# Performance work log

Hardware: AMD Instinct MI355X
Metric: run time of the kernel (lower is better)

Reference implementation:

```python
import jax, jax.numpy as jnp
import numpy as np

DIM = 128  # matches init kwarg `dim`; scale = dim ** 0.5


def setup_inputs() -> dict:
    key = jax.random.key(0)
    k1, k2, k3, k4 = jax.random.split(key, 4)
    A = 100000
    K = 1600000  # num edges
    z_msg_all = jax.random.normal(k1, (A, DIM), dtype=jnp.float32)
    recv_query_all = jax.random.normal(k2, (A, DIM), dtype=jnp.float32)
    i_idx = jax.random.randint(k3, (K,), 0, A, dtype=jnp.int64)
    j_idx = jax.random.randint(k4, (K,), 0, A, dtype=jnp.int64)
    return {"z_msg_all": z_msg_all, "recv_query_all": recv_query_all,
            "i_idx": i_idx, "j_idx": j_idx, "A": A}


def reference(z_msg_all, recv_query_all, i_idx, j_idx, A):
    # q_j = z[j], k_i = z[i]; per-edge scores; segmented softmax over recipient j;
    # weighted scatter-add of values k_i into pooled[j]. recv_query_all is unused
    # in the original forward (kept for signature fidelity).
    scale = DIM ** 0.5
    k = z_msg_all[i_idx]                     # (K, D) gather
    q = z_msg_all[j_idx]                     # (K, D) gather
    scores = jnp.sum(q * k, axis=-1) / scale  # (K,)
    # segmented softmax (3-pass: amax, exp, sum)
    max_per = jax.ops.segment_max(scores, j_idx, num_segments=A)  # (A,)
    exp = jnp.exp(scores - max_per[j_idx])                         # (K,)
    denom = jax.ops.segment_sum(exp, j_idx, num_segments=A)        # (A,)
    alpha = exp / (denom[j_idx] + 1e-6)                            # (K,)
    # weighted scatter-add of values into recipients
    pooled = jax.ops.segment_sum(alpha[:, None] * k, j_idx, num_segments=A)  # (A, D)
    return pooled
```

## Files before the change

kernel.cpp:

```cpp
#include <hip/hip_runtime.h>
#include <math.h>


typedef _Float16 h2 __attribute__((ext_vector_type(2)));

#define CAP   8192
#define ABLK  512
#define EPB   2048

__device__ inline h2 as_h2(unsigned u) { return __builtin_bit_cast(h2, u); }

__global__ __launch_bounds__(ABLK) void bin_kernel(
        const float* __restrict__ z, uint4* __restrict__ z16,
        const int* __restrict__ i_idx, const int* __restrict__ j_idx,
        int* __restrict__ gcount, unsigned* __restrict__ binned,
        int n16, int K, int NB) {
    int tid = threadIdx.x;

    {
        const float4* __restrict__ z4 = reinterpret_cast<const float4*>(z);
        int nth = gridDim.x * ABLK;
        for (int t = blockIdx.x * ABLK + tid; t < n16; t += nth) {
            float4 a = z4[(size_t)2 * t];
            float4 c = z4[(size_t)2 * t + 1];
            uint4 o;
            o.x = __builtin_bit_cast(unsigned, __builtin_amdgcn_cvt_pkrtz(a.x, a.y));
            o.y = __builtin_bit_cast(unsigned, __builtin_amdgcn_cvt_pkrtz(a.z, a.w));
            o.z = __builtin_bit_cast(unsigned, __builtin_amdgcn_cvt_pkrtz(c.x, c.y));
            o.w = __builtin_bit_cast(unsigned, __builtin_amdgcn_cvt_pkrtz(c.z, c.w));
            z16[t] = o;
        }
    }

    __shared__ int lhist[ABLK];
    __shared__ int loff[ABLK + 1];
    __shared__ int lcur[ABLK];
    __shared__ int gbase[ABLK];
    __shared__ unsigned staged_p[EPB];
    __shared__ unsigned short staged_b[EPB];

    lhist[tid] = 0;
    __syncthreads();

    int ebase = blockIdx.x * EPB;
    int myi[4], myj[4], myb[4];
    #pragma unroll
    for (int q = 0; q < 4; ++q) {
        int e = ebase + tid + q * ABLK;
        if (e < K) {
            myj[q] = j_idx[e];
            myi[q] = i_idx[e];
            myb[q] = myj[q] >> 8;
            atomicAdd(&lhist[myb[q]], 1);
        } else {
            myb[q] = -1;
        }
    }
    __syncthreads();
    for (int off = 1; off < ABLK; off <<= 1) {
        int v = (tid >= off) ? lhist[tid - off] : 0;
        __syncthreads();
        lhist[tid] += v;
        __syncthreads();
    }
    loff[tid + 1] = lhist[tid];
    if (tid == 0) loff[0] = 0;
    __syncthreads();
    int cntb = loff[tid + 1] - loff[tid];
    if (tid < NB && cntb > 0)
        gbase[tid] = tid * CAP + atomicAdd(&gcount[tid], cntb);
    lcur[tid] = loff[tid];
    __syncthreads();
    #pragma unroll
    for (int q = 0; q < 4; ++q) {
        if (myb[q] >= 0) {
            int p = atomicAdd(&lcur[myb[q]], 1);
            staged_p[p] = ((unsigned)myi[q] << 8) | ((unsigned)myj[q] & 255u);
            staged_b[p] = (unsigned short)myb[q];
        }
    }
    __syncthreads();
    int totE = loff[ABLK];
    for (int idx = tid; idx < totE; idx += ABLK) {
        int bb = staged_b[idx];
        binned[(size_t)gbase[bb] + (idx - loff[bb])] = staged_p[idx];
    }
}

__global__ __launch_bounds__(512) void finish_kernel(
        unsigned* __restrict__ binned, const int* __restrict__ gcount,
        int2* __restrict__ seg, int A) {
    __shared__ unsigned staged[CAP];
    __shared__ int hist[256];
    __shared__ int offs[257];
    __shared__ int cur[256];

    int b = blockIdx.x;
    int tid = threadIdx.x;
    int cnt = gcount[b];
    if (cnt > CAP) cnt = CAP;
    unsigned* __restrict__ src = binned + (size_t)b * CAP;

    if (tid < 256) hist[tid] = 0;
    for (int x = tid; x < cnt; x += 512) staged[x] = src[x];
    __syncthreads();
    for (int x = tid; x < cnt; x += 512)
        atomicAdd(&hist[staged[x] & 255u], 1);
    __syncthreads();
    for (int off = 1; off < 256; off <<= 1) {
        int v = 0;
        if (tid < 256 && tid >= off) v = hist[tid - off];
        __syncthreads();
        if (tid < 256 && tid >= off) hist[tid] += v;
        __syncthreads();
    }
    if (tid == 0) offs[0] = 0;
    if (tid < 256) offs[tid + 1] = hist[tid];
    __syncthreads();
    if (tid < 256) cur[tid] = offs[tid];
    __syncthreads();
    for (int x = tid; x < cnt; x += 512) {
        unsigned pk = staged[x];
        int p = atomicAdd(&cur[pk & 255u], 1);
        src[p] = pk >> 8;
    }
    if (tid < 256) {
        int j = (b << 8) + tid;
        if (j < A)
            seg[j] = make_int2(b * CAP + offs[tid], b * CAP + offs[tid + 1]);
    }
}

__global__ __launch_bounds__(256, 8) void attn_kernel(
        const uint4* __restrict__ zk,
        const unsigned* __restrict__ sorted_i, const int2* __restrict__ seg,
        float* __restrict__ out, int A) {
    int w = blockIdx.x * 4 + (threadIdx.x >> 6);
    if (w >= A) return;
    int lane = threadIdx.x & 63;
    int g = lane >> 3;
    int r = lane & 7;

    const float kscale = 0.08838834764831843f * 1.4426950408889634f;

    uint4 uq0 = zk[(size_t)w * 16 + r];
    uint4 uq1 = zk[(size_t)w * 16 + 8 + r];
    h2 qh[8];
    qh[0] = as_h2(uq0.x); qh[1] = as_h2(uq0.y);
    qh[2] = as_h2(uq0.z); qh[3] = as_h2(uq0.w);
    qh[4] = as_h2(uq1.x); qh[5] = as_h2(uq1.y);
    qh[6] = as_h2(uq1.z); qh[7] = as_h2(uq1.w);

    int2 s01 = seg[w];

    float l = 0.0f;
    float acc[16];
    #pragma unroll
    for (int d = 0; d < 16; ++d) acc[d] = 0.0f;

    int p = s01.x + g;
    int i_next = (int)sorted_i[p];
    while (p < s01.y) {
        int i = i_next;
        i_next = (int)sorted_i[p + 8];
        uint4 u0 = zk[(size_t)i * 16 + r];
        uint4 u1 = zk[(size_t)i * 16 + 8 + r];
        h2 kh[8];
        kh[0] = as_h2(u0.x); kh[1] = as_h2(u0.y);
        kh[2] = as_h2(u0.z); kh[3] = as_h2(u0.w);
        kh[4] = as_h2(u1.x); kh[5] = as_h2(u1.y);
        kh[6] = as_h2(u1.z); kh[7] = as_h2(u1.w);

        float pa = __builtin_amdgcn_fdot2(qh[0], kh[0], 0.0f, false);
        float pb = __builtin_amdgcn_fdot2(qh[4], kh[4], 0.0f, false);
        pa = __builtin_amdgcn_fdot2(qh[1], kh[1], pa, false);
        pb = __builtin_amdgcn_fdot2(qh[5], kh[5], pb, false);
        pa = __builtin_amdgcn_fdot2(qh[2], kh[2], pa, false);
        pb = __builtin_amdgcn_fdot2(qh[6], kh[6], pb, false);
        pa = __builtin_amdgcn_fdot2(qh[3], kh[3], pa, false);
        pb = __builtin_amdgcn_fdot2(qh[7], kh[7], pb, false);
        float part = pa + pb;
        part += __shfl_xor(part, 1);
        part += __shfl_xor(part, 2);
        part += __shfl_xor(part, 4);

        float pe = exp2f(part * kscale);
        l += pe;
        #pragma unroll
        for (int t = 0; t < 8; ++t) {
            acc[2 * t]     = fmaf(pe, (float)kh[t].x, acc[2 * t]);
            acc[2 * t + 1] = fmaf(pe, (float)kh[t].y, acc[2 * t + 1]);
        }
        p += 8;
    }

    l += __shfl_xor(l, 8);
    l += __shfl_xor(l, 16);
    l += __shfl_xor(l, 32);

    {
        bool hi = (g & 4) != 0;
        #pragma unroll
        for (int t = 0; t < 4; ++t) {
            float sx = hi ? acc[2 * t]     : acc[2 * t + 8];
            float sy = hi ? acc[2 * t + 1] : acc[2 * t + 9];
            float rx = __shfl_xor(sx, 32);
            float ry = __shfl_xor(sy, 32);
            float kx = hi ? acc[2 * t + 8] : acc[2 * t];
            float ky = hi ? acc[2 * t + 9] : acc[2 * t + 1];
            acc[2 * t]     = kx + rx;
            acc[2 * t + 1] = ky + ry;
        }
        hi = (g & 2) != 0;
        #pragma unroll
        for (int t = 0; t < 2; ++t) {
            float sx = hi ? acc[2 * t]     : acc[2 * t + 4];
            float sy = hi ? acc[2 * t + 1] : acc[2 * t + 5];
            float rx = __shfl_xor(sx, 16);
            float ry = __shfl_xor(sy, 16);
            float kx = hi ? acc[2 * t + 4] : acc[2 * t];
            float ky = hi ? acc[2 * t + 5] : acc[2 * t + 1];
            acc[2 * t]     = kx + rx;
            acc[2 * t + 1] = ky + ry;
        }
        hi = (g & 1) != 0;
        {
            float sx = hi ? acc[0] : acc[2];
            float sy = hi ? acc[1] : acc[3];
            float rx = __shfl_xor(sx, 8);
            float ry = __shfl_xor(sy, 8);
            float kx = hi ? acc[2] : acc[0];
            float ky = hi ? acc[3] : acc[1];
            acc[0] = kx + rx;
            acc[1] = ky + ry;
        }
    }

    float inv = 1.0f / (l + 1e-6f);
    float2 o;
    o.x = acc[0] * inv;
    o.y = acc[1] * inv;
    int o_idx = ((g & 4) << 3) + 4 * r + (g & 3);
    reinterpret_cast<float2*>(out)[(size_t)w * 64 + o_idx] = o;
}

extern "C" void kernel_launch(void* const* d_in, const int* in_sizes, int n_in,
                              void* d_out, int out_size, void* d_ws, size_t ws_size,
                              hipStream_t stream) {
    const float* z     = (const float*)d_in[0];
    const int*   i_idx = (const int*)d_in[2];
    const int*   j_idx = (const int*)d_in[3];

    const int D = 128;
    int A = in_sizes[0] / D;
    int K = in_sizes[2];
    int n16 = A * (D / 8);
    int NB = (A + 255) >> 8;

    unsigned short* z16 = (unsigned short*)d_ws;
    unsigned* binned = (unsigned*)(z16 + (size_t)A * 128);
    int2* seg = (int2*)(binned + (size_t)NB * CAP);
    int* gcount = (int*)(seg + A);

    float* out = (float*)d_out;

    (void)hipMemsetAsync(gcount, 0, (size_t)NB * sizeof(int), stream);
    bin_kernel<<<(K + EPB - 1) / EPB, ABLK, 0, stream>>>(
        z, (uint4*)z16, i_idx, j_idx, gcount, binned, n16, K, NB);
    finish_kernel<<<NB, 512, 0, stream>>>(binned, gcount, seg, A);
    attn_kernel<<<(A + 3) / 4, 256, 0, stream>>>((const uint4*)z16, binned,
                                                 seg, out, A);
}
```

Baseline: 119.7 us.

## Deepen attn gather prefetch, double edges per bin block, widen finish sort

The attention loop now software-pipelines the fp16 key-row gather one iteration ahead and prefetches the index two iterations ahead, clamping indices so the speculative loads stay in bounds. The binning kernel handles 8 edges per thread instead of 4, uses an unrolled fixed-count conversion loop, and is sized so its grid also covers the fp32-to-fp16 conversion. The finish kernel runs 1024 threads and sorts into shared memory before a coalesced write-back, replacing scattered global writes. These changes aim to hide gather latency and cut launch/scatter costs, at the price of more registers in the attention kernel and more shared memory in finish.

Result: faster. 104.3 us (-12.9%).

```diff
diff --git a/kernel.cpp b/kernel.cpp
--- a/kernel.cpp
+++ b/kernel.cpp
@@ -6,7 +6,7 @@
 
 #define CAP   8192
 #define ABLK  512
-#define EPB   2048
+#define EPB   (ABLK * 8)
 
 __device__ inline h2 as_h2(unsigned u) { return __builtin_bit_cast(h2, u); }
 
@@ -16,19 +16,24 @@
         int* __restrict__ gcount, unsigned* __restrict__ binned,
         int n16, int K, int NB) {
     int tid = threadIdx.x;
+    int t0 = blockIdx.x * ABLK + tid;
+    int nth = gridDim.x * ABLK;
 
     {
         const float4* __restrict__ z4 = reinterpret_cast<const float4*>(z);
-        int nth = gridDim.x * ABLK;
-        for (int t = blockIdx.x * ABLK + tid; t < n16; t += nth) {
-            float4 a = z4[(size_t)2 * t];
-            float4 c = z4[(size_t)2 * t + 1];
-            uint4 o;
-            o.x = __builtin_bit_cast(unsigned, __builtin_amdgcn_cvt_pkrtz(a.x, a.y));
-            o.y = __builtin_bit_cast(unsigned, __builtin_amdgcn_cvt_pkrtz(a.z, a.w));
-            o.z = __builtin_bit_cast(unsigned, __builtin_amdgcn_cvt_pkrtz(c.x, c.y));
-            o.w = __builtin_bit_cast(unsigned, __builtin_amdgcn_cvt_pkrtz(c.z, c.w));
-            z16[t] = o;
+        #pragma unroll
+        for (int q = 0; q < 8; ++q) {
+            int t = t0 + q * nth;
+            if (t < n16) {
+                float4 a = z4[(size_t)2 * t];
+                float4 c = z4[(size_t)2 * t + 1];
+                uint4 o;
+                o.x = __builtin_bit_cast(unsigned, __builtin_amdgcn_cvt_pkrtz(a.x, a.y));
+                o.y = __builtin_bit_cast(unsigned, __builtin_amdgcn_cvt_pkrtz(a.z, a.w));
+                o.z = __builtin_bit_cast(unsigned, __builtin_amdgcn_cvt_pkrtz(c.x, c.y));
+                o.w = __builtin_bit_cast(unsigned, __builtin_amdgcn_cvt_pkrtz(c.z, c.w));
+                z16[t] = o;
+            }
         }
     }
 
@@ -43,9 +48,9 @@
     __syncthreads();
 
     int ebase = blockIdx.x * EPB;
-    int myi[4], myj[4], myb[4];
+    int myi[8], myj[8], myb[8];
     #pragma unroll
-    for (int q = 0; q < 4; ++q) {
+    for (int q = 0; q < 8; ++q) {
         int e = ebase + tid + q * ABLK;
         if (e < K) {
             myj[q] = j_idx[e];
@@ -72,7 +77,7 @@
     lcur[tid] = loff[tid];
     __syncthreads();
     #pragma unroll
-    for (int q = 0; q < 4; ++q) {
+    for (int q = 0; q < 8; ++q) {
         if (myb[q] >= 0) {
             int p = atomicAdd(&lcur[myb[q]], 1);
             staged_p[p] = ((unsigned)myi[q] << 8) | ((unsigned)myj[q] & 255u);
@@ -87,10 +92,11 @@
     }
 }
 
-__global__ __launch_bounds__(512) void finish_kernel(
+__global__ __launch_bounds__(1024) void finish_kernel(
         unsigned* __restrict__ binned, const int* __restrict__ gcount,
         int2* __restrict__ seg, int A) {
     __shared__ unsigned staged[CAP];
+    __shared__ int sorted_loc[CAP];
     __shared__ int hist[256];
     __shared__ int offs[257];
     __shared__ int cur[256];
@@ -102,9 +108,9 @@
     unsigned* __restrict__ src = binned + (size_t)b * CAP;
 
     if (tid < 256) hist[tid] = 0;
-    for (int x = tid; x < cnt; x += 512) staged[x] = src[x];
-    __syncthreads();
-    for (int x = tid; x < cnt; x += 512)
+    for (int x = tid; x < cnt; x += 1024) staged[x] = src[x];
+    __syncthreads();
+    for (int x = tid; x < cnt; x += 1024)
         atomicAdd(&hist[staged[x] & 255u], 1);
     __syncthreads();
     for (int off = 1; off < 256; off <<= 1) {
@@ -119,11 +125,13 @@
     __syncthreads();
     if (tid < 256) cur[tid] = offs[tid];
     __syncthreads();
-    for (int x = tid; x < cnt; x += 512) {
+    for (int x = tid; x < cnt; x += 1024) {
         unsigned pk = staged[x];
         int p = atomicAdd(&cur[pk & 255u], 1);
-        src[p] = pk >> 8;
-    }
+        sorted_loc[p] = (int)(pk >> 8);
+    }
+    __syncthreads();
+    for (int x = tid; x < cnt; x += 1024) src[x] = (unsigned)sorted_loc[x];
     if (tid < 256) {
         int j = (b << 8) + tid;
         if (j < A)
@@ -159,12 +167,19 @@
     for (int d = 0; d < 16; ++d) acc[d] = 0.0f;
 
     int p = s01.x + g;
-    int i_next = (int)sorted_i[p];
+    unsigned i0 = sorted_i[p];
+    i0 = (i0 < (unsigned)A) ? i0 : 0u;
+    uint4 u0 = zk[(size_t)i0 * 16 + r];
+    uint4 u1 = zk[(size_t)i0 * 16 + 8 + r];
+    unsigned i1 = sorted_i[p + 8];
+    i1 = (i1 < (unsigned)A) ? i1 : 0u;
+
     while (p < s01.y) {
-        int i = i_next;
-        i_next = (int)sorted_i[p + 8];
-        uint4 u0 = zk[(size_t)i * 16 + r];
-        uint4 u1 = zk[(size_t)i * 16 + 8 + r];
+        uint4 n0 = zk[(size_t)i1 * 16 + r];
+        uint4 n1 = zk[(size_t)i1 * 16 + 8 + r];
+        unsigned i2 = sorted_i[p + 16];
+        i2 = (i2 < (unsigned)A) ? i2 : 0u;
+
         h2 kh[8];
         kh[0] = as_h2(u0.x); kh[1] = as_h2(u0.y);
         kh[2] = as_h2(u0.z); kh[3] = as_h2(u0.w);
@@ -191,6 +206,7 @@
             acc[2 * t]     = fmaf(pe, (float)kh[t].x, acc[2 * t]);
             acc[2 * t + 1] = fmaf(pe, (float)kh[t].y, acc[2 * t + 1]);
         }
+        u0 = n0; u1 = n1; i1 = i2;
         p += 8;
     }
 
@@ -265,9 +281,12 @@
     float* out = (float*)d_out;
 
     (void)hipMemsetAsync(gcount, 0, (size_t)NB * sizeof(int), stream);
-    bin_kernel<<<(K + EPB - 1) / EPB, ABLK, 0, stream>>>(
-        z, (uint4*)z16, i_idx, j_idx, gcount, binned, n16, K, NB);
-    finish_kernel<<<NB, 512, 0, stream>>>(binned, gcount, seg, A);
+    int gA = (K + EPB - 1) / EPB;
+    int gC = (n16 + EPB - 1) / EPB;
+    if (gC > gA) gA = gC;
+    bin_kernel<<<gA, ABLK, 0, stream>>>(z, (uint4*)z16, i_idx, j_idx,
+                                        gcount, binned, n16, K, NB);
+    finish_kernel<<<NB, 1024, 0, stream>>>(binned, gcount, seg, A);
     attn_kernel<<<(A + 3) / 4, 256, 0, stream>>>((const uint4*)z16, binned,
                                                  seg, out, A);
 }
```
